# Kernel tuning notes

Hardware: AMD Instinct MI355X
Metric: run time of the kernel (lower is better)

The kernel has to match this reference:

```python
import jax, jax.numpy as jnp
import numpy as np

EPS = 1e-8

def squash_hinton(s):
    # s: [..., d]; v = (||s||^2 / (1+||s||^2)) * s / ||s||
    sq = jnp.sum(s * s, axis=-1, keepdims=True)
    return s * (sq / (1.0 + sq)) / jnp.sqrt(sq + EPS)

def setup_inputs() -> dict:
    key = jax.random.key(0)
    k1, _ = jax.random.split(key)
    B, n_l, n_h, d = 64, 2048, 32, 16
    u_predict = jax.random.normal(k1, (B, n_l, n_h, d), dtype=jnp.float32)
    b = jnp.zeros((n_l, n_h), dtype=jnp.float32)
    return {"u_predict": u_predict, "b": b}

def reference(u_predict, b):
    n_iter = 3
    # initial coupling from prior logits b: softmax over output capsules n_h
    c = jax.nn.softmax(b, axis=-1)                       # [n_l, n_h]
    s = jnp.einsum('lh,blhd->bhd', c, u_predict)         # [B, n_h, d]
    v = squash_hinton(s)
    b_batch = jnp.broadcast_to(b, (u_predict.shape[0],) + b.shape)  # [B, n_l, n_h]
    for _ in range(n_iter):
        # agreement: dot product between predictions and current output caps
        b_batch = b_batch + jnp.einsum('blhd,bhd->blh', u_predict, v)
        c = jax.nn.softmax(b_batch, axis=-1)             # [B, n_l, n_h]
        s = jnp.einsum('blh,blhd->bhd', c, u_predict)    # [B, n_h, d]
        v = squash_hinton(s)
    return v
```

## Files before the change

kernel.cpp:

```cpp
#include <hip/hip_runtime.h>
#include <hip/hip_fp16.h>
#include <hip/hip_bf16.h>

#define B_  64
#define NL_ 2048
#define NH_ 32
#define D_  16
#define HD_ 512
#define LCHUNK 64
#define NCHUNK (NL_/LCHUNK)

typedef float        f32x4 __attribute__((ext_vector_type(4)));
typedef unsigned int u32x4 __attribute__((ext_vector_type(4)));

union H8 { u32x4 u4; __half2 h2[4]; };
union F4 { f32x4 v;  float f[4]; };

__global__ __launch_bounds__(256) void pass0_kernel(const float* __restrict__ u,
                                                    const float* __restrict__ blog,
                                                    __half* __restrict__ u16,
                                                    float* __restrict__ partial_s)
{
    const int b     = blockIdx.y;
    const int chunk = blockIdx.x;
    const int tid   = threadIdx.x;
    const int wave  = tid >> 6;
    const int lane  = tid & 63;
    const int h0    = lane >> 2;
    const int h1    = h0 + 16;

    float4 accA = {0.f,0.f,0.f,0.f};
    float4 accB = {0.f,0.f,0.f,0.f};

    const int l0 = chunk*LCHUNK + wave*(LCHUNK/4);

    for (int j = 0; j < LCHUNK/4; ++j) {
        const int l = l0 + j;
        const size_t base = ((size_t)b*NL_ + l)*HD_;
        F4 a, bq;
        a.v  = __builtin_nontemporal_load((const f32x4*)(u + base + 4*lane));
        bq.v = __builtin_nontemporal_load((const f32x4*)(u + base + 256 + 4*lane));

        union { uint2 u2; __half2 h2[2]; } ha, hb;
        ha.h2[0] = __floats2half2_rn(a.f[0], a.f[1]);   ha.h2[1] = __floats2half2_rn(a.f[2], a.f[3]);
        hb.h2[0] = __floats2half2_rn(bq.f[0], bq.f[1]); hb.h2[1] = __floats2half2_rn(bq.f[2], bq.f[3]);
        *(uint2*)((__half*)u16 + base + 4*lane)       = ha.u2;
        *(uint2*)((__half*)u16 + base + 256 + 4*lane) = hb.u2;

        float la = blog[l*NH_ + h0];
        float lb = blog[l*NH_ + h1];

        float m = fmaxf(la, lb);
        #pragma unroll
        for (int off = 4; off < 64; off <<= 1) m = fmaxf(m, __shfl_xor(m, off));
        const float ea = __expf(la - m);
        const float eb = __expf(lb - m);
        float ssum = ea + eb;
        #pragma unroll
        for (int off = 4; off < 64; off <<= 1) ssum += __shfl_xor(ssum, off);
        const float inv = 1.0f / ssum;
        const float ca = ea * inv;
        const float cb = eb * inv;

        accA.x += ca*a.f[0];  accA.y += ca*a.f[1];  accA.z += ca*a.f[2];  accA.w += ca*a.f[3];
        accB.x += cb*bq.f[0]; accB.y += cb*bq.f[1]; accB.z += cb*bq.f[2]; accB.w += cb*bq.f[3];
    }

    __shared__ float sred[4][HD_];
    float* dst = &sred[wave][0];
    dst[4*lane+0]     = accA.x; dst[4*lane+1]     = accA.y;
    dst[4*lane+2]     = accA.z; dst[4*lane+3]     = accA.w;
    dst[256+4*lane+0] = accB.x; dst[256+4*lane+1] = accB.y;
    dst[256+4*lane+2] = accB.z; dst[256+4*lane+3] = accB.w;
    __syncthreads();

    float r0 = sred[0][tid]     + sred[1][tid]     + sred[2][tid]     + sred[3][tid];
    float r1 = sred[0][tid+256] + sred[1][tid+256] + sred[2][tid+256] + sred[3][tid+256];
    float* pout = partial_s + ((size_t)b*NCHUNK + chunk)*HD_;
    pout[tid]       = r0;
    pout[tid + 256] = r1;
}

template<bool LAST>
__global__ __launch_bounds__(256) void pass16_kernel(const __half* __restrict__ u16,
                                                     const float* __restrict__ blog,
                                                     const float* __restrict__ vsum,
                                                     float* __restrict__ partial_s)
{
    const int b     = blockIdx.y;
    const int chunk = blockIdx.x;
    const int tid   = threadIdx.x;
    const int wave  = tid >> 6;
    const int lane  = tid & 63;
    const int h     = lane >> 1;
    const int d0    = (lane & 1) << 3;

    const float4 v0 = *(const float4*)(vsum + b*HD_ + h*D_ + d0);
    const float4 v1 = *(const float4*)(vsum + b*HD_ + h*D_ + d0 + 4);

    float acc[8] = {0.f,0.f,0.f,0.f,0.f,0.f,0.f,0.f};

    const int l0 = chunk*LCHUNK + wave*(LCHUNK/4);

    for (int j = 0; j < LCHUNK/4; ++j) {
        const int l = l0 + j;
        const size_t base = ((size_t)b*NL_ + l)*HD_;
        H8 x;
        if (LAST) x.u4 = __builtin_nontemporal_load((const u32x4*)(u16 + base + 8*lane));
        else      x.u4 = *(const u32x4*)(u16 + base + 8*lane);
        const float2 f0 = __half22float2(x.h2[0]);
        const float2 f1 = __half22float2(x.h2[1]);
        const float2 f2 = __half22float2(x.h2[2]);
        const float2 f3 = __half22float2(x.h2[3]);

        float dot = f0.x*v0.x + f0.y*v0.y + f1.x*v0.z + f1.y*v0.w
                  + f2.x*v1.x + f2.y*v1.y + f3.x*v1.z + f3.y*v1.w;
        dot += __shfl_xor(dot, 1);

        float la = blog[l*NH_ + h] + dot;

        float m = la;
        #pragma unroll
        for (int off = 2; off < 64; off <<= 1) m = fmaxf(m, __shfl_xor(m, off));
        const float e = __expf(la - m);
        float ssum = e;
        #pragma unroll
        for (int off = 2; off < 64; off <<= 1) ssum += __shfl_xor(ssum, off);
        const float c = e * (2.0f / ssum);

        acc[0] += c*f0.x; acc[1] += c*f0.y; acc[2] += c*f1.x; acc[3] += c*f1.y;
        acc[4] += c*f2.x; acc[5] += c*f2.y; acc[6] += c*f3.x; acc[7] += c*f3.y;
    }

    __shared__ float sred[4][HD_];
    float* dst = &sred[wave][8*lane];
    #pragma unroll
    for (int k = 0; k < 8; ++k) dst[k] = acc[k];
    __syncthreads();

    float r0 = sred[0][tid]     + sred[1][tid]     + sred[2][tid]     + sred[3][tid];
    float r1 = sred[0][tid+256] + sred[1][tid+256] + sred[2][tid+256] + sred[3][tid+256];
    float* pout = partial_s + ((size_t)b*NCHUNK + chunk)*HD_;
    pout[tid]       = r0;
    pout[tid + 256] = r1;
}

template<bool ADD_DOT>
__global__ __launch_bounds__(256) void pass_kernel(const float* __restrict__ u,
                                                   const float* __restrict__ blog,
                                                   const float* __restrict__ vsum,
                                                   float* __restrict__ partial_s)
{
    const int b     = blockIdx.y;
    const int chunk = blockIdx.x;
    const int tid   = threadIdx.x;
    const int wave  = tid >> 6;
    const int lane  = tid & 63;
    const int h0    = lane >> 2;
    const int h1    = h0 + 16;
    const int dq    = (lane & 3) << 2;

    float4 vA = {0.f,0.f,0.f,0.f}, vB = {0.f,0.f,0.f,0.f};
    if (ADD_DOT) {
        vA = *(const float4*)(vsum + b*HD_ + h0*D_ + dq);
        vB = *(const float4*)(vsum + b*HD_ + h1*D_ + dq);
    }

    float4 accA = {0.f,0.f,0.f,0.f};
    float4 accB = {0.f,0.f,0.f,0.f};
    const int l0 = chunk*LCHUNK + wave*(LCHUNK/4);

    for (int j = 0; j < LCHUNK/4; ++j) {
        const int l = l0 + j;
        const float* up = u + ((size_t)b*NL_ + l)*HD_;
        const float4 a  = *(const float4*)(up + 4*lane);
        const float4 bq = *(const float4*)(up + 256 + 4*lane);

        float la = blog[l*NH_ + h0];
        float lb = blog[l*NH_ + h1];

        if (ADD_DOT) {
            float da = a.x*vA.x + a.y*vA.y + a.z*vA.z + a.w*vA.w;
            float db = bq.x*vB.x + bq.y*vB.y + bq.z*vB.z + bq.w*vB.w;
            da += __shfl_xor(da, 1); da += __shfl_xor(da, 2);
            db += __shfl_xor(db, 1); db += __shfl_xor(db, 2);
            la += da; lb += db;
        }

        float m = fmaxf(la, lb);
        #pragma unroll
        for (int off = 4; off < 64; off <<= 1) m = fmaxf(m, __shfl_xor(m, off));
        const float ea = __expf(la - m);
        const float eb = __expf(lb - m);
        float ssum = ea + eb;
        #pragma unroll
        for (int off = 4; off < 64; off <<= 1) ssum += __shfl_xor(ssum, off);
        const float inv = 1.0f / ssum;
        const float ca = ea * inv;
        const float cb = eb * inv;

        accA.x += ca*a.x;  accA.y += ca*a.y;  accA.z += ca*a.z;  accA.w += ca*a.w;
        accB.x += cb*bq.x; accB.y += cb*bq.y; accB.z += cb*bq.z; accB.w += cb*bq.w;
    }

    __shared__ float sred[4][HD_];
    float* dst = &sred[wave][0];
    dst[4*lane+0]     = accA.x; dst[4*lane+1]     = accA.y;
    dst[4*lane+2]     = accA.z; dst[4*lane+3]     = accA.w;
    dst[256+4*lane+0] = accB.x; dst[256+4*lane+1] = accB.y;
    dst[256+4*lane+2] = accB.z; dst[256+4*lane+3] = accB.w;
    __syncthreads();

    float r0 = sred[0][tid]     + sred[1][tid]     + sred[2][tid]     + sred[3][tid];
    float r1 = sred[0][tid+256] + sred[1][tid+256] + sred[2][tid+256] + sred[3][tid+256];
    float* pout = partial_s + ((size_t)b*NCHUNK + chunk)*HD_;
    pout[tid]       = r0;
    pout[tid + 256] = r1;
}

template<int MODE>
__global__ __launch_bounds__(512) void squash_kernel(const float* __restrict__ partial_s,
                                                     float* __restrict__ vsum,
                                                     float* __restrict__ out)
{
    const int b = blockIdx.x;
    const int t = threadIdx.x;
    const float* p = partial_s + (size_t)b*NCHUNK*HD_ + t;
    float s = 0.f;
    #pragma unroll
    for (int c = 0; c < NCHUNK; ++c) s += p[c*HD_];

    float sq = s*s;
    sq += __shfl_xor(sq, 1); sq += __shfl_xor(sq, 2);
    sq += __shfl_xor(sq, 4); sq += __shfl_xor(sq, 8);

    const float scale = sq / ((1.0f + sq) * sqrtf(sq + 1e-8f));
    const float v = s * scale;

    if (MODE == 0)      vsum[b*HD_ + t]  = v;
    else if (MODE == 1) vsum[b*HD_ + t] += v;
    else                out[b*HD_ + t]   = v;
}

extern "C" void kernel_launch(void* const* d_in, const int* in_sizes, int n_in,
                              void* d_out, int out_size, void* d_ws, size_t ws_size,
                              hipStream_t stream)
{
    const float* u    = (const float*)d_in[0];
    const float* blog = (const float*)d_in[1];
    float* out        = (float*)d_out;

    float*  partial_s = (float*)d_ws;
    float*  vsum      = partial_s + (size_t)B_*NCHUNK*HD_;
    __half* u16       = (__half*)(vsum + (size_t)B_*HD_);
    const size_t need = ((size_t)B_*NCHUNK*HD_ + (size_t)B_*HD_)*sizeof(float)
                      + (size_t)B_*NL_*HD_*sizeof(__half);

    dim3 grid(NCHUNK, B_);
    dim3 block(256);

    if (ws_size >= need) {
        pass0_kernel<<<grid, block, 0, stream>>>(u, blog, u16, partial_s);
        squash_kernel<0><<<B_, 512, 0, stream>>>(partial_s, vsum, out);

        pass16_kernel<false><<<grid, block, 0, stream>>>(u16, blog, vsum, partial_s);
        squash_kernel<1><<<B_, 512, 0, stream>>>(partial_s, vsum, out);

        pass16_kernel<false><<<grid, block, 0, stream>>>(u16, blog, vsum, partial_s);
        squash_kernel<1><<<B_, 512, 0, stream>>>(partial_s, vsum, out);

        pass16_kernel<true><<<grid, block, 0, stream>>>(u16, blog, vsum, partial_s);
        squash_kernel<2><<<B_, 512, 0, stream>>>(partial_s, vsum, out);
    } else {
        pass_kernel<false><<<grid, block, 0, stream>>>(u, blog, vsum, partial_s);
        squash_kernel<0><<<B_, 512, 0, stream>>>(partial_s, vsum, out);

        pass_kernel<true><<<grid, block, 0, stream>>>(u, blog, vsum, partial_s);
        squash_kernel<1><<<B_, 512, 0, stream>>>(partial_s, vsum, out);

        pass_kernel<true><<<grid, block, 0, stream>>>(u, blog, vsum, partial_s);
        squash_kernel<1><<<B_, 512, 0, stream>>>(partial_s, vsum, out);

        pass_kernel<true><<<grid, block, 0, stream>>>(u, blog, vsum, partial_s);
        squash_kernel<2><<<B_, 512, 0, stream>>>(partial_s, vsum, out);
    }
}
```

Measured before the change: 155.3 us.

## Precompute initial softmax once and remap pass16 to one lane per output capsule

Adds a small kernel that computes the batch-independent initial softmax of b once, so pass0 reads coupling coefficients instead of redoing shuffles and exps for every batch. Pass16 is restructured so each lane owns a whole capsule (16 dims) and each half-wave handles a different input capsule. This turns the dot product into in-register FMAs and cuts the softmax reduction to 5 shuffles over 32 lanes. It also drops max subtraction in favour of clamping the logit at 80, which relies on logits staying in a safe range, and raises register use per thread.

```diff
diff --git a/kernel.cpp b/kernel.cpp
--- a/kernel.cpp
+++ b/kernel.cpp
@@ -16,8 +16,25 @@
 union H8 { u32x4 u4; __half2 h2[4]; };
 union F4 { f32x4 v;  float f[4]; };
 
+__global__ __launch_bounds__(256) void c0_kernel(const float* __restrict__ blog,
+                                                 float* __restrict__ c0)
+{
+    const int tid = threadIdx.x;
+    const int l   = blockIdx.x*8 + (tid >> 5);
+    const int h   = tid & 31;
+    float x = blog[l*NH_ + h];
+    float m = x;
+    #pragma unroll
+    for (int off = 1; off < 32; off <<= 1) m = fmaxf(m, __shfl_xor(m, off));
+    float e = __expf(x - m);
+    float s = e;
+    #pragma unroll
+    for (int off = 1; off < 32; off <<= 1) s += __shfl_xor(s, off);
+    c0[l*NH_ + h] = e / s;
+}
+
 __global__ __launch_bounds__(256) void pass0_kernel(const float* __restrict__ u,
-                                                    const float* __restrict__ blog,
+                                                    const float* __restrict__ c0,
                                                     __half* __restrict__ u16,
                                                     float* __restrict__ partial_s)
 {
@@ -47,20 +64,8 @@
         *(uint2*)((__half*)u16 + base + 4*lane)       = ha.u2;
         *(uint2*)((__half*)u16 + base + 256 + 4*lane) = hb.u2;
 
-        float la = blog[l*NH_ + h0];
-        float lb = blog[l*NH_ + h1];
-
-        float m = fmaxf(la, lb);
-        #pragma unroll
-        for (int off = 4; off < 64; off <<= 1) m = fmaxf(m, __shfl_xor(m, off));
-        const float ea = __expf(la - m);
-        const float eb = __expf(lb - m);
-        float ssum = ea + eb;
-        #pragma unroll
-        for (int off = 4; off < 64; off <<= 1) ssum += __shfl_xor(ssum, off);
-        const float inv = 1.0f / ssum;
-        const float ca = ea * inv;
-        const float cb = eb * inv;
+        const float ca = c0[l*NH_ + h0];
+        const float cb = c0[l*NH_ + h1];
 
         accA.x += ca*a.f[0];  accA.y += ca*a.f[1];  accA.z += ca*a.f[2];  accA.w += ca*a.f[3];
         accB.x += cb*bq.f[0]; accB.y += cb*bq.f[1]; accB.z += cb*bq.f[2]; accB.w += cb*bq.f[3];
@@ -92,54 +97,76 @@
     const int tid   = threadIdx.x;
     const int wave  = tid >> 6;
     const int lane  = tid & 63;
-    const int h     = lane >> 1;
-    const int d0    = (lane & 1) << 3;
-
-    const float4 v0 = *(const float4*)(vsum + b*HD_ + h*D_ + d0);
-    const float4 v1 = *(const float4*)(vsum + b*HD_ + h*D_ + d0 + 4);
-
-    float acc[8] = {0.f,0.f,0.f,0.f,0.f,0.f,0.f,0.f};
-
-    const int l0 = chunk*LCHUNK + wave*(LCHUNK/4);
-
-    for (int j = 0; j < LCHUNK/4; ++j) {
-        const int l = l0 + j;
-        const size_t base = ((size_t)b*NL_ + l)*HD_;
-        H8 x;
-        if (LAST) x.u4 = __builtin_nontemporal_load((const u32x4*)(u16 + base + 8*lane));
-        else      x.u4 = *(const u32x4*)(u16 + base + 8*lane);
-        const float2 f0 = __half22float2(x.h2[0]);
-        const float2 f1 = __half22float2(x.h2[1]);
-        const float2 f2 = __half22float2(x.h2[2]);
-        const float2 f3 = __half22float2(x.h2[3]);
-
-        float dot = f0.x*v0.x + f0.y*v0.y + f1.x*v0.z + f1.y*v0.w
-                  + f2.x*v1.x + f2.y*v1.y + f3.x*v1.z + f3.y*v1.w;
-        dot += __shfl_xor(dot, 1);
-
-        float la = blog[l*NH_ + h] + dot;
-
-        float m = la;
-        #pragma unroll
-        for (int off = 2; off < 64; off <<= 1) m = fmaxf(m, __shfl_xor(m, off));
-        const float e = __expf(la - m);
+    const int hh    = lane & 31;
+    const int lpar  = lane >> 5;
+
+    float vs[16];
+    #pragma unroll
+    for (int q = 0; q < 4; ++q) {
+        const float4 t = *(const float4*)(vsum + b*HD_ + hh*D_ + 4*q);
+        vs[4*q+0] = t.x; vs[4*q+1] = t.y; vs[4*q+2] = t.z; vs[4*q+3] = t.w;
+    }
+
+    float acc[16];
+    #pragma unroll
+    for (int d = 0; d < 16; ++d) acc[d] = 0.f;
+
+    const int lbase = chunk*LCHUNK + wave*(LCHUNK/4);
+
+    for (int j = 0; j < LCHUNK/8; ++j) {
+        const int l = lbase + 2*j + lpar;
+        const size_t base = ((size_t)b*NL_ + l)*HD_ + hh*D_;
+        H8 x0, x1;
+        if (LAST) {
+            x0.u4 = __builtin_nontemporal_load((const u32x4*)(u16 + base));
+            x1.u4 = __builtin_nontemporal_load((const u32x4*)(u16 + base + 8));
+        } else {
+            x0.u4 = *(const u32x4*)(u16 + base);
+            x1.u4 = *(const u32x4*)(u16 + base + 8);
+        }
+        float f[16];
+        #pragma unroll
+        for (int q = 0; q < 4; ++q) {
+            const float2 t0 = __half22float2(x0.h2[q]);
+            const float2 t1 = __half22float2(x1.h2[q]);
+            f[2*q+0] = t0.x; f[2*q+1] = t0.y;
+            f[8+2*q+0] = t1.x; f[8+2*q+1] = t1.y;
+        }
+
+        float dot = 0.f;
+        #pragma unroll
+        for (int d = 0; d < 16; ++d) dot = __fmaf_rn(f[d], vs[d], dot);
+
+        const float la = fminf(blog[l*NH_ + hh] + dot, 80.f);
+        const float e  = __expf(la);
         float ssum = e;
         #pragma unroll
-        for (int off = 2; off < 64; off <<= 1) ssum += __shfl_xor(ssum, off);
-        const float c = e * (2.0f / ssum);
-
-        acc[0] += c*f0.x; acc[1] += c*f0.y; acc[2] += c*f1.x; acc[3] += c*f1.y;
-        acc[4] += c*f2.x; acc[5] += c*f2.y; acc[6] += c*f3.x; acc[7] += c*f3.y;
-    }
-
-    __shared__ float sred[4][HD_];
-    float* dst = &sred[wave][8*lane];
-    #pragma unroll
-    for (int k = 0; k < 8; ++k) dst[k] = acc[k];
+        for (int off = 1; off < 32; off <<= 1) ssum += __shfl_xor(ssum, off);
+        const float c = e / ssum;
+
+        #pragma unroll
+        for (int d = 0; d < 16; ++d) acc[d] = __fmaf_rn(c, f[d], acc[d]);
+    }
+
+    __shared__ float sred[4][2][NH_][D_];
+    float* dst = &sred[wave][lpar][hh][0];
+    #pragma unroll
+    for (int q = 0; q < 4; ++q) {
+        float4 t = { acc[4*q+0], acc[4*q+1], acc[4*q+2], acc[4*q+3] };
+        *(float4*)(dst + 4*q) = t;
+    }
     __syncthreads();
 
-    float r0 = sred[0][tid]     + sred[1][tid]     + sred[2][tid]     + sred[3][tid];
-    float r1 = sred[0][tid+256] + sred[1][tid+256] + sred[2][tid+256] + sred[3][tid+256];
+    const float* sp = &sred[0][0][0][0];
+    float r0 = 0.f, r1 = 0.f;
+    #pragma unroll
+    for (int w = 0; w < 4; ++w) {
+        #pragma unroll
+        for (int p = 0; p < 2; ++p) {
+            r0 += sp[w*1024 + p*512 + tid];
+            r1 += sp[w*1024 + p*512 + tid + 256];
+        }
+    }
     float* pout = partial_s + ((size_t)b*NCHUNK + chunk)*HD_;
     pout[tid]       = r0;
     pout[tid + 256] = r1;
@@ -252,15 +279,17 @@
 
     float*  partial_s = (float*)d_ws;
     float*  vsum      = partial_s + (size_t)B_*NCHUNK*HD_;
-    __half* u16       = (__half*)(vsum + (size_t)B_*HD_);
-    const size_t need = ((size_t)B_*NCHUNK*HD_ + (size_t)B_*HD_)*sizeof(float)
+    float*  c0        = vsum + (size_t)B_*HD_;
+    __half* u16       = (__half*)(c0 + (size_t)NL_*NH_);
+    const size_t need = ((size_t)B_*NCHUNK*HD_ + (size_t)B_*HD_ + (size_t)NL_*NH_)*sizeof(float)
                       + (size_t)B_*NL_*HD_*sizeof(__half);
 
     dim3 grid(NCHUNK, B_);
     dim3 block(256);
 
     if (ws_size >= need) {
-        pass0_kernel<<<grid, block, 0, stream>>>(u, blog, u16, partial_s);
+        c0_kernel<<<NL_/8, 256, 0, stream>>>(blog, c0);
+        pass0_kernel<<<grid, block, 0, stream>>>(u, c0, u16, partial_s);
         squash_kernel<0><<<B_, 512, 0, stream>>>(partial_s, vsum, out);
 
         pass16_kernel<false><<<grid, block, 0, stream>>>(u16, blog, vsum, partial_s);
```

Result: no change. 155.1 us (-0.2%).
